# Optimization experiments

Hardware: AMD Instinct MI355X
Metric: run time of the kernel (lower is better)

Reference implementation:

```python
import jax, jax.numpy as jnp
import numpy as np

# ---- static config (mirrors init_kwargs) ----
WIN_X, WIN_Y = 12, 12
GRID_X, GRID_Y = 468, 468
BATCH = 4
SHIFTS = ((0, 0), (6, 6))
MAX_WIN_X = GRID_X // WIN_X + 1            # 40
MAX_WIN_Y = GRID_Y // WIN_Y + 1            # 40
MAX_WIN_PER_SAMPLE = MAX_WIN_X * MAX_WIN_Y # 1600
# (level, max_tokens, drop_range_lo, drop_range_hi)
DROP_INFO = ((0, 30, 0, 30), (1, 60, 30, 60), (2, 100, 60, 100000))
SENTINEL = 2_000_000_000  # window id for masked-out voxels (sorts to the end)


def _window_partition(coors):
    # coors: [N,4] = [b, z, y, x] int32 -> batch-unique window index per shift
    out = []
    for sx, sy in SHIFTS:
        x = coors[:, 3] + sx
        y = coors[:, 2] + sy
        wx = x // WIN_X
        wy = y // WIN_Y
        out.append((coors[:, 0] * MAX_WIN_PER_SAMPLE + wx * MAX_WIN_Y + wy).astype(jnp.int32))
    return out


def _sort_group_stats(win):
    # inner index within each equal-value group (counting-sort style) and group size per element
    order = jnp.argsort(win)                      # stable
    s = win[order]
    n = win.shape[0]
    left_s = jnp.searchsorted(s, s, side='left')
    inner_sorted = jnp.arange(n, dtype=win.dtype) - left_s.astype(win.dtype)
    inner = jnp.zeros_like(win).at[order].set(inner_sorted)
    counts = (jnp.searchsorted(s, win, side='right') - jnp.searchsorted(s, win, side='left')).astype(win.dtype)
    return inner, counts


def _drop_single_shift(win, valid):
    # equivalent of SSTInputLayer.drop_single_shift restricted to `valid` voxels
    w = jnp.where(valid, win, SENTINEL)
    inner, counts = _sort_group_stats(w)
    target = jnp.zeros_like(w)
    lvl = -jnp.ones_like(w)
    for dl, max_tok, lo, hi in DROP_INFO:
        m = (counts >= lo) & (counts < hi)
        target = jnp.where(m, max_tok, target)
        lvl = jnp.where(m, dl, lvl)
    keep = valid & (inner < target)
    return keep, jnp.where(valid, lvl, -1)


def _make_continuous(w):
    # dense-rank of window ids (make_continuous_inds) over a sentinel-masked array
    order = jnp.argsort(w)
    s = w[order]
    new_grp = jnp.concatenate([jnp.zeros((1,), w.dtype), (s[1:] != s[:-1]).astype(w.dtype)])
    rank = jnp.cumsum(new_grp)
    return jnp.zeros_like(w).at[order].set(rank)


def _flat2win(win, keep, lvl):
    # per-voxel position in the [num_windows, max_tokens] buffer of its drop level; -1 if dropped
    out = -jnp.ones_like(win)
    for dl, max_tok, _, _ in DROP_INFO:
        valid = keep & (lvl == dl)
        w = jnp.where(valid, win, SENTINEL)
        conti = _make_continuous(w)
        inner, _ = _sort_group_stats(w)
        out = jnp.where(valid, conti * max_tok + inner, out)
    return out


def reference(voxel_feat, coors):
    coors = coors.astype(jnp.int32)
    bwi0, bwi1 = _window_partition(coors)
    n = voxel_feat.shape[0]
    all_valid = jnp.ones((n,), bool)
    keep0, lvl0 = _drop_single_shift(bwi0, all_valid)
    keep1, lvl1 = _drop_single_shift(bwi1, keep0)   # shift-1 drop computed among shift-0 survivors
    keep = keep0 & keep1
    feat = jnp.where(keep[:, None], voxel_feat, 0.0)  # fixed-shape analogue of voxel_feat[voxel_keep_inds]
    f2w0 = _flat2win(bwi0, keep, lvl0)
    f2w1 = _flat2win(bwi1, keep, lvl1)
    return feat, keep, lvl0, lvl1, bwi0, bwi1, f2w0, f2w1


def setup_inputs() -> dict:
    key = jax.random.key(0)
    k1, k2, k3, k4 = jax.random.split(key, 4)
    n, c = 300000, 128
    voxel_feat = jax.random.normal(k1, (n, c), dtype=jnp.float32)
    b = jax.random.randint(k2, (n,), 0, BATCH)
    y = jax.random.randint(k3, (n,), 0, GRID_Y)
    x = jax.random.randint(k4, (n,), 0, GRID_X)
    z = jnp.zeros((n,), jnp.int32)
    coors = jnp.stack([b, z, y, x], axis=1).astype(jnp.int32)
    return {"voxel_feat": voxel_feat, "coors": coors}
```

## Files before the change

### kernel.cpp

```cpp
#include <hip/hip_runtime.h>


#define NWIN 6400
#define CAP 128

__device__ __forceinline__ int targ_of(int k) {
    return (k < 30) ? 30 : (k < 60) ? 60 : (k < 100000) ? 100 : 0;
}
__device__ __forceinline__ int lvl_of(int k) {
    return (k < 30) ? 0 : (k < 60) ? 1 : (k < 100000) ? 2 : -1;
}

__global__ void k_zero(int* __restrict__ z) {
    int i = blockIdx.x * 256 + threadIdx.x;
    if (i < 3 * NWIN + 1) z[i] = 0;
}

__global__ void __launch_bounds__(256) k_winscat(
    const int4* __restrict__ c4, int n,
    int* __restrict__ w0a, int* __restrict__ w1a,
    int* __restrict__ cnt0, int* __restrict__ seg0) {
    int i = blockIdx.x * 256 + threadIdx.x;
    if (i >= n) return;
    int4 c = c4[i];
    int w0 = c.x * 1600 + (c.w / 12) * 40 + (c.z / 12);
    int w1 = c.x * 1600 + ((c.w + 6) / 12) * 40 + ((c.z + 6) / 12);
    w0a[i] = w0;
    w1a[i] = w1;
    int p = atomicAdd(&cnt0[w0], 1);
    if (p < CAP) seg0[w0 * CAP + p] = i;
}

__global__ void __launch_bounds__(256) k_rank0(
    const int* __restrict__ cnt0, const int* __restrict__ seg0,
    const int* __restrict__ w0a, const int* __restrict__ w1a, int n,
    int* __restrict__ keep0, int* __restrict__ rk0,
    int* __restrict__ cnt1, int* __restrict__ seg1) {
    int w = blockIdx.x * 4 + (threadIdx.x >> 6);
    int lane = threadIdx.x & 63;
    int k = cnt0[w];
    if (k == 0) return;
    int target = targ_of(k);
    const int* s = seg0 + w * CAP;
    if (k <= 64) {
        int v = (lane < k) ? s[lane] : 0x7FFFFFFF;
        int r = 0;
        for (int j = 0; j < k; j++) { int b = __shfl(v, j, 64); r += (b < v) ? 1 : 0; }
        if (lane < k) {
            int kp = (r < target) ? 1 : 0;
            keep0[v] = kp;
            if (kp) {
                rk0[v] = r;
                int w1 = w1a[v];
                int p = atomicAdd(&cnt1[w1], 1);
                if (p < CAP) seg1[w1 * CAP + p] = v;
            }
        }
    } else if (k <= CAP) {
        int k2 = k - 64;
        int v0 = s[lane];
        int v1 = (lane < k2) ? s[64 + lane] : 0x7FFFFFFF;
        int r0 = 0, r1 = 0;
        for (int j = 0; j < 64; j++) { int b = __shfl(v0, j, 64); r0 += (b < v0); r1 += (b < v1); }
        for (int j = 0; j < k2; j++) { int b = __shfl(v1, j, 64); r0 += (b < v0); r1 += (b < v1); }
        {
            int kp = (r0 < target) ? 1 : 0;
            keep0[v0] = kp;
            if (kp) {
                rk0[v0] = r0;
                int w1 = w1a[v0]; int p = atomicAdd(&cnt1[w1], 1);
                if (p < CAP) seg1[w1 * CAP + p] = v0;
            }
        }
        if (lane < k2) {
            int kp = (r1 < target) ? 1 : 0;
            keep0[v1] = kp;
            if (kp) {
                rk0[v1] = r1;
                int w1 = w1a[v1]; int p = atomicAdd(&cnt1[w1], 1);
                if (p < CAP) seg1[w1 * CAP + p] = v1;
            }
        }
    } else {
        if (lane == 0) {
            int c = 0;
            for (int i = 0; i < n; i++) {
                if (w0a[i] == w) {
                    int kp = (c < target) ? 1 : 0;
                    keep0[i] = kp;
                    if (kp) {
                        rk0[i] = c;
                        int w1 = w1a[i]; int p = atomicAdd(&cnt1[w1], 1);
                        if (p < CAP) seg1[w1 * CAP + p] = i;
                    }
                    c++;
                }
            }
        }
    }
}

__global__ void __launch_bounds__(256) k_rank1(
    const int* __restrict__ cnt1, const int* __restrict__ seg1,
    const int* __restrict__ w0a, const int* __restrict__ w1a,
    const int* __restrict__ keep0, int n,
    int* __restrict__ keepF, int* __restrict__ rk1,
    int* __restrict__ keptC1, int* __restrict__ keptC0,
    int* __restrict__ dropCnt, int* __restrict__ droplist) {
    int w = blockIdx.x * 4 + (threadIdx.x >> 6);
    int lane = threadIdx.x & 63;
    int k = cnt1[w];
    int target = targ_of(k);
    if (lane == 0) keptC1[w] = (k < target) ? k : target;
    if (k == 0) return;
    const int* s = seg1 + w * CAP;
    if (k <= 64) {
        int v = (lane < k) ? s[lane] : 0x7FFFFFFF;
        int r = 0;
        for (int j = 0; j < k; j++) { int b = __shfl(v, j, 64); r += (b < v) ? 1 : 0; }
        if (lane < k) {
            int kp = (r < target) ? 1 : 0;
            keepF[v] = kp;
            if (kp) { rk1[v] = r; atomicAdd(&keptC0[w0a[v]], 1); }
            else    { int d = atomicAdd(dropCnt, 1); droplist[d] = v; }
        }
    } else if (k <= CAP) {
        int k2 = k - 64;
        int v0 = s[lane];
        int v1 = (lane < k2) ? s[64 + lane] : 0x7FFFFFFF;
        int r0 = 0, r1 = 0;
        for (int j = 0; j < 64; j++) { int b = __shfl(v0, j, 64); r0 += (b < v0); r1 += (b < v1); }
        for (int j = 0; j < k2; j++) { int b = __shfl(v1, j, 64); r0 += (b < v0); r1 += (b < v1); }
        {
            int kp = (r0 < target) ? 1 : 0;
            keepF[v0] = kp;
            if (kp) { rk1[v0] = r0; atomicAdd(&keptC0[w0a[v0]], 1); }
            else    { int d = atomicAdd(dropCnt, 1); droplist[d] = v0; }
        }
        if (lane < k2) {
            int kp = (r1 < target) ? 1 : 0;
            keepF[v1] = kp;
            if (kp) { rk1[v1] = r1; atomicAdd(&keptC0[w0a[v1]], 1); }
            else    { int d = atomicAdd(dropCnt, 1); droplist[d] = v1; }
        }
    } else {
        if (lane == 0) {
            int c = 0;
            for (int i = 0; i < n; i++) {
                if (w1a[i] == w && keep0[i]) {
                    int kp = (c < target) ? 1 : 0;
                    keepF[i] = kp;
                    if (kp) { rk1[i] = c; atomicAdd(&keptC0[w0a[i]], 1); }
                    else    { int d = atomicAdd(dropCnt, 1); droplist[d] = i; }
                    c++;
                }
            }
        }
    }
}

__device__ __forceinline__ void conti_scan(
    const int* __restrict__ cnt, const int* __restrict__ keptC,
    int* __restrict__ conti, int* pc0, int* pc1, int* pc2) {
    int t = threadIdx.x;
    int st = t * 25;
    int c0 = 0, c1 = 0, c2 = 0;
    for (int j = 0; j < 25; j++) {
        int w = st + j;
        if (keptC[w] > 0) {
            int l = lvl_of(cnt[w]);
            c0 += (l == 0); c1 += (l == 1); c2 += (l == 2);
        }
    }
    pc0[t] = c0; pc1[t] = c1; pc2[t] = c2;
    __syncthreads();
    if (t == 0) {
        int a = 0, b = 0, c = 0;
        for (int j = 0; j < 256; j++) {
            int v0 = pc0[j], v1 = pc1[j], v2 = pc2[j];
            pc0[j] = a; pc1[j] = b; pc2[j] = c;
            a += v0; b += v1; c += v2;
        }
    }
    __syncthreads();
    int a0 = pc0[t], a1 = pc1[t], a2 = pc2[t];
    for (int j = 0; j < 25; j++) {
        int w = st + j;
        int l = lvl_of(cnt[w]);
        conti[w] = (l == 0) ? a0 : (l == 1) ? a1 : (l == 2) ? a2 : 0;
        if (keptC[w] > 0) {
            if (l == 0) a0++; else if (l == 1) a1++; else if (l == 2) a2++;
        }
    }
}

__global__ void k_fix(
    const int* __restrict__ cnt0, const int* __restrict__ keptC0, int* __restrict__ conti0,
    const int* __restrict__ cnt1, const int* __restrict__ keptC1, int* __restrict__ conti1,
    const int* __restrict__ dropCnt, const int* __restrict__ droplist,
    const int* __restrict__ w0a, const int* __restrict__ seg0,
    const int* __restrict__ keep0, const int* __restrict__ keepF,
    int* __restrict__ rk0, int n) {
    __shared__ int pc0[256], pc1[256], pc2[256];
    if (blockIdx.x == 0) { conti_scan(cnt0, keptC0, conti0, pc0, pc1, pc2); return; }
    if (blockIdx.x == 1) { conti_scan(cnt1, keptC1, conti1, pc0, pc1, pc2); return; }
    int nd = *dropCnt;
    if (nd == 0) return;
    int waveId = (blockIdx.x - 2) * 4 + (threadIdx.x >> 6);
    int nWaves = (gridDim.x - 2) * 4;
    int lane = threadIdx.x & 63;
    for (int e = waveId; e < nd; e += nWaves) {
        int u = droplist[e];
        int w = w0a[u];
        int k = cnt0[w];
        if (k <= CAP) {
            const int* s = seg0 + w * CAP;
            for (int j = lane; j < k; j += 64) {
                int v = s[j];
                if (v > u && keep0[v] && keepF[v]) atomicSub(&rk0[v], 1);
            }
        } else if (lane == 0) {
            for (int i = u + 1; i < n; i++) {
                if (w0a[i] == w && keep0[i] && keepF[i]) atomicSub(&rk0[i], 1);
            }
        }
    }
}

__global__ void __launch_bounds__(256) k_finalfeat(
    int n, const int* __restrict__ w0a, const int* __restrict__ w1a,
    const int* __restrict__ keep0, const int* __restrict__ keepF,
    const int* __restrict__ cnt0, const int* __restrict__ cnt1,
    const int* __restrict__ conti0, const int* __restrict__ conti1,
    const int* __restrict__ rk0, const int* __restrict__ rk1,
    const float4* __restrict__ feat, float* __restrict__ out, int nbScalar) {
    if ((int)blockIdx.x < nbScalar) {
        int i = blockIdx.x * 256 + threadIdx.x;
        if (i >= n) return;
        size_t N = (size_t)n;
        float* o = out + N * 128;
        int w0 = w0a[i], w1 = w1a[i];
        int k0 = keep0[i];
        int kf = (k0 && keepF[i]) ? 1 : 0;
        int l0 = lvl_of(cnt0[w0]);
        int l1 = k0 ? lvl_of(cnt1[w1]) : -1;
        int f0 = -1, f1 = -1;
        if (kf) {
            int mt0 = (l0 == 0) ? 30 : (l0 == 1) ? 60 : 100;
            int mt1 = (l1 == 0) ? 30 : (l1 == 1) ? 60 : 100;
            f0 = conti0[w0] * mt0 + rk0[i];
            f1 = conti1[w1] * mt1 + rk1[i];
        }
        o[i]         = (float)kf;
        o[N + i]     = (float)l0;
        o[2 * N + i] = (float)l1;
        o[3 * N + i] = (float)w0;
        o[4 * N + i] = (float)w1;
        o[5 * N + i] = (float)f0;
        o[6 * N + i] = (float)f1;
    } else {
        int gid = (blockIdx.x - nbScalar) * 256 + threadIdx.x;
        int total = n * 32;
        if (gid >= total) return;
        int row = gid >> 5;
        float4 v = feat[gid];
        if (!(keep0[row] && keepF[row])) { v.x = 0.f; v.y = 0.f; v.z = 0.f; v.w = 0.f; }
        ((float4*)out)[gid] = v;
    }
}

extern "C" void kernel_launch(void* const* d_in, const int* in_sizes, int n_in,
                              void* d_out, int out_size, void* d_ws, size_t ws_size,
                              hipStream_t stream) {
    (void)n_in; (void)out_size; (void)ws_size;
    const float* feat = (const float*)d_in[0];
    const int* coors  = (const int*)d_in[1];
    int n = in_sizes[1] / 4;
    float* out = (float*)d_out;
    int* ws = (int*)d_ws;

    int* cnt0     = ws;
    int* cnt1     = ws + 6400;
    int* keptC0   = ws + 12800;
    int* dropCnt  = ws + 19200;
    int* keptC1   = ws + 25600;
    int* conti0   = ws + 32000;
    int* conti1   = ws + 38400;
    int* droplist = ws + 44800;
    int* w0a      = droplist + n;
    int* w1a      = w0a + n;
    int* keep0    = w1a + n;
    int* keepF    = keep0 + n;
    int* rk0      = keepF + n;
    int* rk1      = rk0 + n;
    int* seg0     = rk1 + n;
    int* seg1     = seg0 + NWIN * CAP;

    int nb = (n + 255) / 256;
    int fb = (n * 32 + 255) / 256;

    k_zero<<<(3 * NWIN + 1 + 255) / 256, 256, 0, stream>>>(cnt0);
    k_winscat<<<nb, 256, 0, stream>>>((const int4*)coors, n, w0a, w1a, cnt0, seg0);
    k_rank0<<<NWIN / 4, 256, 0, stream>>>(cnt0, seg0, w0a, w1a, n,
                                          keep0, rk0, cnt1, seg1);
    k_rank1<<<NWIN / 4, 256, 0, stream>>>(cnt1, seg1, w0a, w1a, keep0, n,
                                          keepF, rk1, keptC1, keptC0,
                                          dropCnt, droplist);
    k_fix<<<66, 256, 0, stream>>>(cnt0, keptC0, conti0, cnt1, keptC1, conti1,
                                  dropCnt, droplist, w0a, seg0, keep0, keepF,
                                  rk0, n);
    k_finalfeat<<<nb + fb, 256, 0, stream>>>(n, w0a, w1a, keep0, keepF, cnt0, cnt1,
                                             conti0, conti1, rk0, rk1,
                                             (const float4*)feat, out, nb);
}
```

Baseline: 390.2 us.

## Copy features early and fuse fix with finalize via in-kernel completion counter

The feature copy moves into the first scatter kernel as an unconditional nontemporal copy. Dropped rows are zeroed later by the finalize threads, so the big copy no longer waits on the keep masks. The conti scan and rank-fix work are merged with the scalar finalize into one kernel. Blocks get roles through an atomic ticket, and finalize blocks spin on a done counter. This removes one launch and the serialized feature pass at the end, but it relies on the worker blocks being resident and adds scattered per-row zero writes.

New measurement: 442.6 us. +13.4%, slower.

```diff
diff --git a/kernel.cpp b/kernel.cpp
--- a/kernel.cpp
+++ b/kernel.cpp
@@ -3,6 +3,9 @@
 
 #define NWIN 6400
 #define CAP 128
+#define FIXB 30
+
+typedef float f4 __attribute__((ext_vector_type(4)));
 
 __device__ __forceinline__ int targ_of(int k) {
     return (k < 30) ? 30 : (k < 60) ? 60 : (k < 100000) ? 100 : 0;
@@ -13,14 +16,24 @@
 
 __global__ void k_zero(int* __restrict__ z) {
     int i = blockIdx.x * 256 + threadIdx.x;
-    if (i < 3 * NWIN + 1) z[i] = 0;
-}
-
-__global__ void __launch_bounds__(256) k_winscat(
+    if (i < 3 * NWIN + 3) z[i] = 0;
+}
+
+__global__ void __launch_bounds__(256) k_copyscat(
     const int4* __restrict__ c4, int n,
     int* __restrict__ w0a, int* __restrict__ w1a,
-    int* __restrict__ cnt0, int* __restrict__ seg0) {
-    int i = blockIdx.x * 256 + threadIdx.x;
+    int* __restrict__ cnt0, int* __restrict__ seg0,
+    const f4* __restrict__ feat, f4* __restrict__ out, int fb) {
+    int b = blockIdx.x;
+    if (b < fb) {
+        int gid = b * 256 + threadIdx.x;
+        if (gid < n * 32) {
+            f4 v = __builtin_nontemporal_load(&feat[gid]);
+            __builtin_nontemporal_store(v, &out[gid]);
+        }
+        return;
+    }
+    int i = (b - fb) * 256 + threadIdx.x;
     if (i >= n) return;
     int4 c = c4[i];
     int w0 = c.x * 1600 + (c.w / 12) * 40 + (c.z / 12);
@@ -194,79 +207,93 @@
     }
 }
 
-__global__ void k_fix(
-    const int* __restrict__ cnt0, const int* __restrict__ keptC0, int* __restrict__ conti0,
-    const int* __restrict__ cnt1, const int* __restrict__ keptC1, int* __restrict__ conti1,
-    const int* __restrict__ dropCnt, const int* __restrict__ droplist,
-    const int* __restrict__ w0a, const int* __restrict__ seg0,
-    const int* __restrict__ keep0, const int* __restrict__ keepF,
-    int* __restrict__ rk0, int n) {
-    __shared__ int pc0[256], pc1[256], pc2[256];
-    if (blockIdx.x == 0) { conti_scan(cnt0, keptC0, conti0, pc0, pc1, pc2); return; }
-    if (blockIdx.x == 1) { conti_scan(cnt1, keptC1, conti1, pc0, pc1, pc2); return; }
-    int nd = *dropCnt;
-    if (nd == 0) return;
-    int waveId = (blockIdx.x - 2) * 4 + (threadIdx.x >> 6);
-    int nWaves = (gridDim.x - 2) * 4;
-    int lane = threadIdx.x & 63;
-    for (int e = waveId; e < nd; e += nWaves) {
-        int u = droplist[e];
-        int w = w0a[u];
-        int k = cnt0[w];
-        if (k <= CAP) {
-            const int* s = seg0 + w * CAP;
-            for (int j = lane; j < k; j += 64) {
-                int v = s[j];
-                if (v > u && keep0[v] && keepF[v]) atomicSub(&rk0[v], 1);
-            }
-        } else if (lane == 0) {
-            for (int i = u + 1; i < n; i++) {
-                if (w0a[i] == w && keep0[i] && keepF[i]) atomicSub(&rk0[i], 1);
-            }
-        }
-    }
-}
-
-__global__ void __launch_bounds__(256) k_finalfeat(
-    int n, const int* __restrict__ w0a, const int* __restrict__ w1a,
+__global__ void __launch_bounds__(256) k_fixfinal(
+    int n,
+    const int* __restrict__ w0a, const int* __restrict__ w1a,
     const int* __restrict__ keep0, const int* __restrict__ keepF,
     const int* __restrict__ cnt0, const int* __restrict__ cnt1,
-    const int* __restrict__ conti0, const int* __restrict__ conti1,
-    const int* __restrict__ rk0, const int* __restrict__ rk1,
-    const float4* __restrict__ feat, float* __restrict__ out, int nbScalar) {
-    if ((int)blockIdx.x < nbScalar) {
-        int i = blockIdx.x * 256 + threadIdx.x;
-        if (i >= n) return;
-        size_t N = (size_t)n;
-        float* o = out + N * 128;
-        int w0 = w0a[i], w1 = w1a[i];
-        int k0 = keep0[i];
-        int kf = (k0 && keepF[i]) ? 1 : 0;
-        int l0 = lvl_of(cnt0[w0]);
-        int l1 = k0 ? lvl_of(cnt1[w1]) : -1;
-        int f0 = -1, f1 = -1;
-        if (kf) {
-            int mt0 = (l0 == 0) ? 30 : (l0 == 1) ? 60 : 100;
-            int mt1 = (l1 == 0) ? 30 : (l1 == 1) ? 60 : 100;
-            f0 = conti0[w0] * mt0 + rk0[i];
-            f1 = conti1[w1] * mt1 + rk1[i];
-        }
-        o[i]         = (float)kf;
-        o[N + i]     = (float)l0;
-        o[2 * N + i] = (float)l1;
-        o[3 * N + i] = (float)w0;
-        o[4 * N + i] = (float)w1;
-        o[5 * N + i] = (float)f0;
-        o[6 * N + i] = (float)f1;
+    const int* __restrict__ keptC0, const int* __restrict__ keptC1,
+    int* __restrict__ conti0, int* __restrict__ conti1,
+    int* __restrict__ rk0, const int* __restrict__ rk1,
+    const int* __restrict__ dropCnt, const int* __restrict__ droplist,
+    const int* __restrict__ seg0,
+    int* __restrict__ roleCtr, int* __restrict__ doneCtr,
+    float* __restrict__ out) {
+    __shared__ int roleSh;
+    __shared__ int pc0[256], pc1[256], pc2[256];
+    if (threadIdx.x == 0) roleSh = atomicAdd(roleCtr, 1);
+    __syncthreads();
+    int role = roleSh;
+
+    if (role < 2) {
+        if (role == 0) conti_scan(cnt0, keptC0, conti0, pc0, pc1, pc2);
+        else           conti_scan(cnt1, keptC1, conti1, pc0, pc1, pc2);
+        __syncthreads();
+        if (threadIdx.x == 0)
+            __hip_atomic_fetch_add(doneCtr, 1, __ATOMIC_RELEASE, __HIP_MEMORY_SCOPE_AGENT);
+        return;
+    }
+    if (role < 2 + FIXB) {
+        int nd = *dropCnt;
+        if (nd > 0) {
+            int waveId = (role - 2) * 4 + (threadIdx.x >> 6);
+            int lane = threadIdx.x & 63;
+            for (int e = waveId; e < nd; e += FIXB * 4) {
+                int u = droplist[e];
+                int w = w0a[u];
+                int k = cnt0[w];
+                if (k <= CAP) {
+                    const int* s = seg0 + w * CAP;
+                    for (int j = lane; j < k; j += 64) {
+                        int v = s[j];
+                        if (v > u && keep0[v] && keepF[v]) atomicSub(&rk0[v], 1);
+                    }
+                } else if (lane == 0) {
+                    for (int i2 = u + 1; i2 < n; i2++)
+                        if (w0a[i2] == w && keep0[i2] && keepF[i2]) atomicSub(&rk0[i2], 1);
+                }
+            }
+        }
+        __syncthreads();
+        if (threadIdx.x == 0)
+            __hip_atomic_fetch_add(doneCtr, 1, __ATOMIC_RELEASE, __HIP_MEMORY_SCOPE_AGENT);
+        return;
+    }
+
+    if (threadIdx.x == 0) {
+        while (__hip_atomic_load(doneCtr, __ATOMIC_RELAXED, __HIP_MEMORY_SCOPE_AGENT) < 2 + FIXB)
+            __builtin_amdgcn_s_sleep(8);
+    }
+    __syncthreads();
+    (void)__hip_atomic_load(doneCtr, __ATOMIC_ACQUIRE, __HIP_MEMORY_SCOPE_AGENT);
+
+    int i = (role - 2 - FIXB) * 256 + threadIdx.x;
+    if (i >= n) return;
+    size_t N = (size_t)n;
+    float* o = out + N * 128;
+    int w0 = w0a[i], w1 = w1a[i];
+    int k0 = keep0[i];
+    int kf = (k0 && keepF[i]) ? 1 : 0;
+    int l0 = lvl_of(cnt0[w0]);
+    int l1 = k0 ? lvl_of(cnt1[w1]) : -1;
+    int f0 = -1, f1 = -1;
+    if (kf) {
+        int mt0 = (l0 == 0) ? 30 : (l0 == 1) ? 60 : 100;
+        int mt1 = (l1 == 0) ? 30 : (l1 == 1) ? 60 : 100;
+        f0 = conti0[w0] * mt0 + rk0[i];
+        f1 = conti1[w1] * mt1 + rk1[i];
     } else {
-        int gid = (blockIdx.x - nbScalar) * 256 + threadIdx.x;
-        int total = n * 32;
-        if (gid >= total) return;
-        int row = gid >> 5;
-        float4 v = feat[gid];
-        if (!(keep0[row] && keepF[row])) { v.x = 0.f; v.y = 0.f; v.z = 0.f; v.w = 0.f; }
-        ((float4*)out)[gid] = v;
-    }
+        f4* row = (f4*)out + (size_t)i * 32;
+        f4 zz = {0.f, 0.f, 0.f, 0.f};
+        for (int j = 0; j < 32; j++) row[j] = zz;
+    }
+    o[i]         = (float)kf;
+    o[N + i]     = (float)l0;
+    o[2 * N + i] = (float)l1;
+    o[3 * N + i] = (float)w0;
+    o[4 * N + i] = (float)w1;
+    o[5 * N + i] = (float)f0;
+    o[6 * N + i] = (float)f1;
 }
 
 extern "C" void kernel_launch(void* const* d_in, const int* in_sizes, int n_in,
@@ -283,6 +310,8 @@
     int* cnt1     = ws + 6400;
     int* keptC0   = ws + 12800;
     int* dropCnt  = ws + 19200;
+    int* roleCtr  = ws + 19201;
+    int* doneCtr  = ws + 19202;
     int* keptC1   = ws + 25600;
     int* conti0   = ws + 32000;
     int* conti1   = ws + 38400;
@@ -299,17 +328,18 @@
     int nb = (n + 255) / 256;
     int fb = (n * 32 + 255) / 256;
 
-    k_zero<<<(3 * NWIN + 1 + 255) / 256, 256, 0, stream>>>(cnt0);
-    k_winscat<<<nb, 256, 0, stream>>>((const int4*)coors, n, w0a, w1a, cnt0, seg0);
+    k_zero<<<(3 * NWIN + 3 + 255) / 256, 256, 0, stream>>>(cnt0);
+    k_copyscat<<<fb + nb, 256, 0, stream>>>((const int4*)coors, n, w0a, w1a,
+                                            cnt0, seg0, (const f4*)feat,
+                                            (f4*)out, fb);
     k_rank0<<<NWIN / 4, 256, 0, stream>>>(cnt0, seg0, w0a, w1a, n,
                                           keep0, rk0, cnt1, seg1);
     k_rank1<<<NWIN / 4, 256, 0, stream>>>(cnt1, seg1, w0a, w1a, keep0, n,
                                           keepF, rk1, keptC1, keptC0,
                                           dropCnt, droplist);
-    k_fix<<<66, 256, 0, stream>>>(cnt0, keptC0, conti0, cnt1, keptC1, conti1,
-                                  dropCnt, droplist, w0a, seg0, keep0, keepF,
-                                  rk0, n);
-    k_finalfeat<<<nb + fb, 256, 0, stream>>>(n, w0a, w1a, keep0, keepF, cnt0, cnt1,
-                                             conti0, conti1, rk0, rk1,
-                                             (const float4*)feat, out, nb);
-}
+    k_fixfinal<<<2 + FIXB + nb, 256, 0, stream>>>(n, w0a, w1a, keep0, keepF,
+                                                  cnt0, cnt1, keptC0, keptC1,
+                                                  conti0, conti1, rk0, rk1,
+                                                  dropCnt, droplist, seg0,
+                                                  roleCtr, doneCtr, out);
+}
```

## Encode keep flags in rank arrays and pack window ids as int2

Applied to the files above, without the earlier changes.

Removes the separate keep0/keepF arrays by initialising rk0/rk1 to -1 and using rank>=0 as the keep flag, and packs the two window ids per voxel into one int2 array. This cuts global memory traffic and scattered writes across rank, fix and final kernels. It adds a -1 fill of 2n ints in the zero kernel and also reduces the k_fix grid from 66 to 34 blocks. The feature copy dominates bandwidth, so the savings act on the smaller metadata paths.

Measured after the change: 377.8 us. 1.03x faster.

```diff
diff --git a/kernel.cpp b/kernel.cpp
--- a/kernel.cpp
+++ b/kernel.cpp
@@ -3,6 +3,7 @@
 
 #define NWIN 6400
 #define CAP 128
+#define HDRN (3 * NWIN + 1)
 
 __device__ __forceinline__ int targ_of(int k) {
     return (k < 30) ? 30 : (k < 60) ? 60 : (k < 100000) ? 100 : 0;
@@ -11,31 +12,30 @@
     return (k < 30) ? 0 : (k < 60) ? 1 : (k < 100000) ? 2 : -1;
 }
 
-__global__ void k_zero(int* __restrict__ z) {
+__global__ void k_zero(int* __restrict__ hdr, int* __restrict__ rkbuf, int n2) {
     int i = blockIdx.x * 256 + threadIdx.x;
-    if (i < 3 * NWIN + 1) z[i] = 0;
+    if (i < HDRN) hdr[i] = 0;
+    if (i < n2) rkbuf[i] = -1;
 }
 
 __global__ void __launch_bounds__(256) k_winscat(
-    const int4* __restrict__ c4, int n,
-    int* __restrict__ w0a, int* __restrict__ w1a,
+    const int4* __restrict__ c4, int n, int2* __restrict__ wp,
     int* __restrict__ cnt0, int* __restrict__ seg0) {
     int i = blockIdx.x * 256 + threadIdx.x;
     if (i >= n) return;
     int4 c = c4[i];
     int w0 = c.x * 1600 + (c.w / 12) * 40 + (c.z / 12);
     int w1 = c.x * 1600 + ((c.w + 6) / 12) * 40 + ((c.z + 6) / 12);
-    w0a[i] = w0;
-    w1a[i] = w1;
+    int2 p2; p2.x = w0; p2.y = w1;
+    wp[i] = p2;
     int p = atomicAdd(&cnt0[w0], 1);
     if (p < CAP) seg0[w0 * CAP + p] = i;
 }
 
 __global__ void __launch_bounds__(256) k_rank0(
     const int* __restrict__ cnt0, const int* __restrict__ seg0,
-    const int* __restrict__ w0a, const int* __restrict__ w1a, int n,
-    int* __restrict__ keep0, int* __restrict__ rk0,
-    int* __restrict__ cnt1, int* __restrict__ seg1) {
+    const int2* __restrict__ wp, int n,
+    int* __restrict__ rk0, int* __restrict__ cnt1, int* __restrict__ seg1) {
     int w = blockIdx.x * 4 + (threadIdx.x >> 6);
     int lane = threadIdx.x & 63;
     int k = cnt0[w];
@@ -46,15 +46,11 @@
         int v = (lane < k) ? s[lane] : 0x7FFFFFFF;
         int r = 0;
         for (int j = 0; j < k; j++) { int b = __shfl(v, j, 64); r += (b < v) ? 1 : 0; }
-        if (lane < k) {
-            int kp = (r < target) ? 1 : 0;
-            keep0[v] = kp;
-            if (kp) {
-                rk0[v] = r;
-                int w1 = w1a[v];
-                int p = atomicAdd(&cnt1[w1], 1);
-                if (p < CAP) seg1[w1 * CAP + p] = v;
-            }
+        if (lane < k && r < target) {
+            rk0[v] = r;
+            int w1 = wp[v].y;
+            int p = atomicAdd(&cnt1[w1], 1);
+            if (p < CAP) seg1[w1 * CAP + p] = v;
         }
     } else if (k <= CAP) {
         int k2 = k - 64;
@@ -63,34 +59,24 @@
         int r0 = 0, r1 = 0;
         for (int j = 0; j < 64; j++) { int b = __shfl(v0, j, 64); r0 += (b < v0); r1 += (b < v1); }
         for (int j = 0; j < k2; j++) { int b = __shfl(v1, j, 64); r0 += (b < v0); r1 += (b < v1); }
-        {
-            int kp = (r0 < target) ? 1 : 0;
-            keep0[v0] = kp;
-            if (kp) {
-                rk0[v0] = r0;
-                int w1 = w1a[v0]; int p = atomicAdd(&cnt1[w1], 1);
-                if (p < CAP) seg1[w1 * CAP + p] = v0;
-            }
-        }
-        if (lane < k2) {
-            int kp = (r1 < target) ? 1 : 0;
-            keep0[v1] = kp;
-            if (kp) {
-                rk0[v1] = r1;
-                int w1 = w1a[v1]; int p = atomicAdd(&cnt1[w1], 1);
-                if (p < CAP) seg1[w1 * CAP + p] = v1;
-            }
+        if (r0 < target) {
+            rk0[v0] = r0;
+            int w1 = wp[v0].y; int p = atomicAdd(&cnt1[w1], 1);
+            if (p < CAP) seg1[w1 * CAP + p] = v0;
+        }
+        if (lane < k2 && r1 < target) {
+            rk0[v1] = r1;
+            int w1 = wp[v1].y; int p = atomicAdd(&cnt1[w1], 1);
+            if (p < CAP) seg1[w1 * CAP + p] = v1;
         }
     } else {
         if (lane == 0) {
             int c = 0;
             for (int i = 0; i < n; i++) {
-                if (w0a[i] == w) {
-                    int kp = (c < target) ? 1 : 0;
-                    keep0[i] = kp;
-                    if (kp) {
+                if (wp[i].x == w) {
+                    if (c < target) {
                         rk0[i] = c;
-                        int w1 = w1a[i]; int p = atomicAdd(&cnt1[w1], 1);
+                        int w1 = wp[i].y; int p = atomicAdd(&cnt1[w1], 1);
                         if (p < CAP) seg1[w1 * CAP + p] = i;
                     }
                     c++;
@@ -102,10 +88,8 @@
 
 __global__ void __launch_bounds__(256) k_rank1(
     const int* __restrict__ cnt1, const int* __restrict__ seg1,
-    const int* __restrict__ w0a, const int* __restrict__ w1a,
-    const int* __restrict__ keep0, int n,
-    int* __restrict__ keepF, int* __restrict__ rk1,
-    int* __restrict__ keptC1, int* __restrict__ keptC0,
+    const int2* __restrict__ wp, const int* __restrict__ rk0, int n,
+    int* __restrict__ rk1, int* __restrict__ keptC1, int* __restrict__ keptC0,
     int* __restrict__ dropCnt, int* __restrict__ droplist) {
     int w = blockIdx.x * 4 + (threadIdx.x >> 6);
     int lane = threadIdx.x & 63;
@@ -119,10 +103,8 @@
         int r = 0;
         for (int j = 0; j < k; j++) { int b = __shfl(v, j, 64); r += (b < v) ? 1 : 0; }
         if (lane < k) {
-            int kp = (r < target) ? 1 : 0;
-            keepF[v] = kp;
-            if (kp) { rk1[v] = r; atomicAdd(&keptC0[w0a[v]], 1); }
-            else    { int d = atomicAdd(dropCnt, 1); droplist[d] = v; }
+            if (r < target) { rk1[v] = r; atomicAdd(&keptC0[wp[v].x], 1); }
+            else            { int d = atomicAdd(dropCnt, 1); droplist[d] = v; }
         }
     } else if (k <= CAP) {
         int k2 = k - 64;
@@ -131,27 +113,19 @@
         int r0 = 0, r1 = 0;
         for (int j = 0; j < 64; j++) { int b = __shfl(v0, j, 64); r0 += (b < v0); r1 += (b < v1); }
         for (int j = 0; j < k2; j++) { int b = __shfl(v1, j, 64); r0 += (b < v0); r1 += (b < v1); }
-        {
-            int kp = (r0 < target) ? 1 : 0;
-            keepF[v0] = kp;
-            if (kp) { rk1[v0] = r0; atomicAdd(&keptC0[w0a[v0]], 1); }
-            else    { int d = atomicAdd(dropCnt, 1); droplist[d] = v0; }
-        }
+        if (r0 < target) { rk1[v0] = r0; atomicAdd(&keptC0[wp[v0].x], 1); }
+        else             { int d = atomicAdd(dropCnt, 1); droplist[d] = v0; }
         if (lane < k2) {
-            int kp = (r1 < target) ? 1 : 0;
-            keepF[v1] = kp;
-            if (kp) { rk1[v1] = r1; atomicAdd(&keptC0[w0a[v1]], 1); }
-            else    { int d = atomicAdd(dropCnt, 1); droplist[d] = v1; }
+            if (r1 < target) { rk1[v1] = r1; atomicAdd(&keptC0[wp[v1].x], 1); }
+            else             { int d = atomicAdd(dropCnt, 1); droplist[d] = v1; }
         }
     } else {
         if (lane == 0) {
             int c = 0;
             for (int i = 0; i < n; i++) {
-                if (w1a[i] == w && keep0[i]) {
-                    int kp = (c < target) ? 1 : 0;
-                    keepF[i] = kp;
-                    if (kp) { rk1[i] = c; atomicAdd(&keptC0[w0a[i]], 1); }
-                    else    { int d = atomicAdd(dropCnt, 1); droplist[d] = i; }
+                if (wp[i].y == w && rk0[i] >= 0) {
+                    if (c < target) { rk1[i] = c; atomicAdd(&keptC0[wp[i].x], 1); }
+                    else            { int d = atomicAdd(dropCnt, 1); droplist[d] = i; }
                     c++;
                 }
             }
@@ -198,9 +172,8 @@
     const int* __restrict__ cnt0, const int* __restrict__ keptC0, int* __restrict__ conti0,
     const int* __restrict__ cnt1, const int* __restrict__ keptC1, int* __restrict__ conti1,
     const int* __restrict__ dropCnt, const int* __restrict__ droplist,
-    const int* __restrict__ w0a, const int* __restrict__ seg0,
-    const int* __restrict__ keep0, const int* __restrict__ keepF,
-    int* __restrict__ rk0, int n) {
+    const int2* __restrict__ wp, const int* __restrict__ seg0,
+    const int* __restrict__ rk1, int* __restrict__ rk0, int n) {
     __shared__ int pc0[256], pc1[256], pc2[256];
     if (blockIdx.x == 0) { conti_scan(cnt0, keptC0, conti0, pc0, pc1, pc2); return; }
     if (blockIdx.x == 1) { conti_scan(cnt1, keptC1, conti1, pc0, pc1, pc2); return; }
@@ -211,45 +184,45 @@
     int lane = threadIdx.x & 63;
     for (int e = waveId; e < nd; e += nWaves) {
         int u = droplist[e];
-        int w = w0a[u];
+        int w = wp[u].x;
         int k = cnt0[w];
         if (k <= CAP) {
             const int* s = seg0 + w * CAP;
             for (int j = lane; j < k; j += 64) {
                 int v = s[j];
-                if (v > u && keep0[v] && keepF[v]) atomicSub(&rk0[v], 1);
+                if (v > u && rk1[v] >= 0) atomicSub(&rk0[v], 1);
             }
         } else if (lane == 0) {
-            for (int i = u + 1; i < n; i++) {
-                if (w0a[i] == w && keep0[i] && keepF[i]) atomicSub(&rk0[i], 1);
-            }
+            for (int i = u + 1; i < n; i++)
+                if (wp[i].x == w && rk1[i] >= 0) atomicSub(&rk0[i], 1);
         }
     }
 }
 
 __global__ void __launch_bounds__(256) k_finalfeat(
-    int n, const int* __restrict__ w0a, const int* __restrict__ w1a,
-    const int* __restrict__ keep0, const int* __restrict__ keepF,
+    int n, const int2* __restrict__ wp,
+    const int* __restrict__ rk0, const int* __restrict__ rk1,
     const int* __restrict__ cnt0, const int* __restrict__ cnt1,
     const int* __restrict__ conti0, const int* __restrict__ conti1,
-    const int* __restrict__ rk0, const int* __restrict__ rk1,
     const float4* __restrict__ feat, float* __restrict__ out, int nbScalar) {
     if ((int)blockIdx.x < nbScalar) {
         int i = blockIdx.x * 256 + threadIdx.x;
         if (i >= n) return;
         size_t N = (size_t)n;
         float* o = out + N * 128;
-        int w0 = w0a[i], w1 = w1a[i];
-        int k0 = keep0[i];
-        int kf = (k0 && keepF[i]) ? 1 : 0;
+        int2 ww = wp[i];
+        int w0 = ww.x, w1 = ww.y;
+        int r0 = rk0[i], r1 = rk1[i];
+        int k0 = (r0 >= 0) ? 1 : 0;
+        int kf = (r1 >= 0) ? 1 : 0;
         int l0 = lvl_of(cnt0[w0]);
         int l1 = k0 ? lvl_of(cnt1[w1]) : -1;
         int f0 = -1, f1 = -1;
         if (kf) {
             int mt0 = (l0 == 0) ? 30 : (l0 == 1) ? 60 : 100;
             int mt1 = (l1 == 0) ? 30 : (l1 == 1) ? 60 : 100;
-            f0 = conti0[w0] * mt0 + rk0[i];
-            f1 = conti1[w1] * mt1 + rk1[i];
+            f0 = conti0[w0] * mt0 + r0;
+            f1 = conti1[w1] * mt1 + r1;
         }
         o[i]         = (float)kf;
         o[N + i]     = (float)l0;
@@ -264,7 +237,7 @@
         if (gid >= total) return;
         int row = gid >> 5;
         float4 v = feat[gid];
-        if (!(keep0[row] && keepF[row])) { v.x = 0.f; v.y = 0.f; v.z = 0.f; v.w = 0.f; }
+        if (rk1[row] < 0) { v.x = 0.f; v.y = 0.f; v.z = 0.f; v.w = 0.f; }
         ((float4*)out)[gid] = v;
     }
 }
@@ -279,6 +252,8 @@
     float* out = (float*)d_out;
     int* ws = (int*)d_ws;
 
+    int nAl = (n + 1) & ~1;
+
     int* cnt0     = ws;
     int* cnt1     = ws + 6400;
     int* keptC0   = ws + 12800;
@@ -287,29 +262,25 @@
     int* conti0   = ws + 32000;
     int* conti1   = ws + 38400;
     int* droplist = ws + 44800;
-    int* w0a      = droplist + n;
-    int* w1a      = w0a + n;
-    int* keep0    = w1a + n;
-    int* keepF    = keep0 + n;
-    int* rk0      = keepF + n;
+    int2* wp      = (int2*)(droplist + nAl);
+    int* rk0      = (int*)wp + 2 * nAl;
     int* rk1      = rk0 + n;
     int* seg0     = rk1 + n;
     int* seg1     = seg0 + NWIN * CAP;
 
     int nb = (n + 255) / 256;
     int fb = (n * 32 + 255) / 256;
-
-    k_zero<<<(3 * NWIN + 1 + 255) / 256, 256, 0, stream>>>(cnt0);
-    k_winscat<<<nb, 256, 0, stream>>>((const int4*)coors, n, w0a, w1a, cnt0, seg0);
-    k_rank0<<<NWIN / 4, 256, 0, stream>>>(cnt0, seg0, w0a, w1a, n,
-                                          keep0, rk0, cnt1, seg1);
-    k_rank1<<<NWIN / 4, 256, 0, stream>>>(cnt1, seg1, w0a, w1a, keep0, n,
-                                          keepF, rk1, keptC1, keptC0,
-                                          dropCnt, droplist);
-    k_fix<<<66, 256, 0, stream>>>(cnt0, keptC0, conti0, cnt1, keptC1, conti1,
-                                  dropCnt, droplist, w0a, seg0, keep0, keepF,
-                                  rk0, n);
-    k_finalfeat<<<nb + fb, 256, 0, stream>>>(n, w0a, w1a, keep0, keepF, cnt0, cnt1,
-                                             conti0, conti1, rk0, rk1,
+    int n2 = 2 * n;
+    int zmax = (n2 > HDRN) ? n2 : HDRN;
+
+    k_zero<<<(zmax + 255) / 256, 256, 0, stream>>>(cnt0, rk0, n2);
+    k_winscat<<<nb, 256, 0, stream>>>((const int4*)coors, n, wp, cnt0, seg0);
+    k_rank0<<<NWIN / 4, 256, 0, stream>>>(cnt0, seg0, wp, n, rk0, cnt1, seg1);
+    k_rank1<<<NWIN / 4, 256, 0, stream>>>(cnt1, seg1, wp, rk0, n,
+                                          rk1, keptC1, keptC0, dropCnt, droplist);
+    k_fix<<<34, 256, 0, stream>>>(cnt0, keptC0, conti0, cnt1, keptC1, conti1,
+                                  dropCnt, droplist, wp, seg0, rk1, rk0, n);
+    k_finalfeat<<<nb + fb, 256, 0, stream>>>(n, wp, rk0, rk1, cnt0, cnt1,
+                                             conti0, conti1,
                                              (const float4*)feat, out, nb);
 }
```
